# Kernel tuning notes

Measured on AMD Instinct MI355X. Metric: run time of the kernel, lower is better.

## Reference

```python
import jax, jax.numpy as jnp
import numpy as np

SPLINE_ORDER = 3
TOP_K = 2
NUM_EXPERTS = 8


def _gram_basis(x, beta_w):
    # x: (B, C, H, W) post-tanh. Returns (B, C*(S+1), H, W).
    P0 = jnp.ones_like(x)
    P1 = x
    ps = [P0, P1]
    for i in range(2, SPLINE_ORDER + 1):
        n, m = i - 1, i
        # beta(n, m) = (m+n)*(m-n)*n^2 / (m^2/(4n^2-1)) * beta_weights[n]
        beta = (m + n) * (m - n) * (n ** 2) * (4.0 * n ** 2 - 1.0) / (m ** 2) * beta_w[n]
        P2 = x * ps[-1] - beta * ps[-2]
        ps.append(P2)
    return jnp.concatenate(ps, axis=1)


def _expert(x, poly_w, beta_w):
    # tanh -> Gram polynomial basis -> SiLU -> conv2d (padding=1, stride=1)
    g = jax.nn.silu(_gram_basis(jnp.tanh(x), beta_w))
    return jax.lax.conv_general_dilated(
        g, poly_w[0], window_strides=(1, 1), padding=[(1, 1), (1, 1)],
        dimension_numbers=('NCHW', 'OIHW', 'NCHW'))


def _cv_squared(v):
    # torch.var is unbiased (ddof=1)
    return jnp.var(v, ddof=1) / (jnp.mean(v) ** 2 + 1e-10)


def reference(x, w_gate, poly_weights, beta_weights):
    B = x.shape[0]
    # gating input: global average pool -> (B, C)
    gate_x = jnp.mean(x, axis=(2, 3))
    probs = jax.nn.softmax(gate_x @ w_gate, axis=1)  # softmax BEFORE topk, as in source
    top_vals, top_idx = jax.lax.top_k(probs, TOP_K + 1)
    tk_vals = top_vals[:, :TOP_K]
    tk_idx = top_idx[:, :TOP_K]
    tk_gates = tk_vals / (jnp.sum(tk_vals, axis=1, keepdims=True) + 1e-6)
    gates = jnp.zeros_like(probs).at[jnp.arange(B)[:, None], tk_idx].set(tk_gates)
    importance = gates.sum(axis=0)
    load = jnp.sum(gates > 0, axis=0).astype(jnp.float32)  # eval-mode load
    loss = (_cv_squared(importance) + _cv_squared(load)) * 0.01
    # All experts share parameters (ModuleList([experts]*num_experts)), so
    # sum_e gates[b,e] * expert_e(x[b]) == gates.sum(1)[b] * expert(x[b]).
    y = _expert(x, poly_weights, beta_weights) * jnp.sum(gates, axis=1)[:, None, None, None]
    return y, loss


def setup_inputs() -> dict:
    key = jax.random.key(0)
    k1, k2, k3, k4 = jax.random.split(key, 4)
    x = jax.random.normal(k1, (16, 32, 192, 192), dtype=jnp.float32)
    w_gate = jax.random.normal(k2, (32, NUM_EXPERTS), dtype=jnp.float32) * 0.1
    poly_weights = jax.random.normal(k3, (1, 32, 32 * (SPLINE_ORDER + 1), 3, 3), dtype=jnp.float32) * 0.05
    beta_weights = jax.random.normal(k4, (SPLINE_ORDER + 1,), dtype=jnp.float32) * 0.01
    return {"x": x, "w_gate": w_gate, "poly_weights": poly_weights, "beta_weights": beta_weights}
```

## Files before the change

### kernel.cpp

```cpp
#include <hip/hip_runtime.h>

typedef unsigned short u16;
typedef unsigned int u32;
typedef __attribute__((ext_vector_type(8))) short bf16x8;
typedef __attribute__((ext_vector_type(4))) float f32x4;

static constexpr int B = 16, C = 32, H = 192, W = 192;
static constexpr int HW = H * W;
static constexpr int E = 8;
static constexpr int CO = 32;
static constexpr int NB = 96;
static constexpr long long NTOT = (long long)B * C * HW;
static constexpr float SILU1 = 0.7310585786300049f;

static constexpr size_t GP_OFF  = (size_t)NTOT * 2;
static constexpr size_t SCL_OFF = GP_OFF + (size_t)B * C * NB * 4;
static constexpr size_t SK_OFF  = SCL_OFF + 128;
static constexpr size_t SS_OFF  = SK_OFF + 288 * 4;
static constexpr size_t WF_OFF  = SS_OFF + 128;

__device__ inline u32 cvt_pk_bf16(float lo, float hi) {
    u32 r;
    asm("v_cvt_pk_bf16_f32 %0, %1, %2" : "=v"(r) : "v"(lo), "v"(hi));
    return r;
}
__device__ inline u16 f2b(float f) {
    u32 u = __float_as_uint(f);
    return (u16)((u + 0x7fffu + ((u >> 16) & 1u)) >> 16);
}
__device__ inline float silu_fast(float z) {
    return z * __builtin_amdgcn_rcpf(1.0f + __expf(-z));
}
__device__ inline float tanh_fast(float z) {
    float e = __expf(2.0f * z);
    return 1.0f - 2.0f * __builtin_amdgcn_rcpf(e + 1.0f);
}

__global__ __launch_bounds__(256) void stage1_prep(const float* __restrict__ x,
                                                   const float* __restrict__ pw,
                                                   u16* __restrict__ t_out,
                                                   float* __restrict__ gpart,
                                                   float* __restrict__ Sk,
                                                   float* __restrict__ Ssum,
                                                   u16* __restrict__ wfrag) {
    __shared__ float sg[2][4][16];
    __shared__ float sred[9][32][8];
    __shared__ float sks[288];
    const int blk = blockIdx.x, tid = threadIdx.x;
    if (blk < B * NB) {
        const int b = blk / NB, band = blk - (blk / NB) * NB;
        const int cp = tid & 15, part = tid >> 4;
        const size_t pbase = (size_t)b * HW + (size_t)(band * 2) * W;
        const float4* xa = (const float4*)(x + (size_t)(b * C + 2 * cp) * HW
                                             + (size_t)(band * 2) * W);
        const float4* xb = (const float4*)(x + (size_t)(b * C + 2 * cp + 1) * HW
                                             + (size_t)(band * 2) * W);
        u32* tw = (u32*)t_out;
        float s0 = 0.0f, s1 = 0.0f;
        #pragma unroll
        for (int k = 0; k < 6; ++k) {
            const int j = k * 16 + part;
            float4 a = xa[j], c = xb[j];
            s0 += (a.x + a.y) + (a.z + a.w);
            s1 += (c.x + c.y) + (c.z + c.w);
            u32 r0 = cvt_pk_bf16(tanh_fast(a.x), tanh_fast(c.x));
            u32 r1 = cvt_pk_bf16(tanh_fast(a.y), tanh_fast(c.y));
            u32 r2 = cvt_pk_bf16(tanh_fast(a.z), tanh_fast(c.z));
            u32 r3 = cvt_pk_bf16(tanh_fast(a.w), tanh_fast(c.w));
            u32* dst = tw + (pbase + (size_t)j * 4) * 16 + cp;
            dst[0] = r0; dst[16] = r1; dst[32] = r2; dst[48] = r3;
        }
        s0 += __shfl_down(s0, 32); s0 += __shfl_down(s0, 16);
        s1 += __shfl_down(s1, 32); s1 += __shfl_down(s1, 16);
        if ((part & 3) == 0) { sg[0][tid >> 6][cp] = s0; sg[1][tid >> 6][cp] = s1; }
        __syncthreads();
        if (tid < 32) {
            const int cpp = tid >> 1, o = tid & 1;
            gpart[(size_t)(b * C + tid) * NB + band] =
                (sg[o][0][cpp] + sg[o][1][cpp]) + (sg[o][2][cpp] + sg[o][3][cpp]);
        }
        return;
    }
    if (blk < B * NB + 108) {
        int j = (blk - B * NB) * 256 + tid;
        int e = j & 7, lane = (j >> 3) & 63, rest = j >> 9;
        int half = rest & 1, pt = rest >> 1;
        int p = pt / 9, tap = pt - p * 9;
        int co = half * 16 + (lane & 15);
        int ci = 32 + p * 32 + (lane >> 4) * 8 + e;
        wfrag[j] = f2b(pw[(size_t)co * 1152 + ci * 9 + tap]);
        return;
    }
    {
        const int co = tid & 31, sub = tid >> 5;
        #pragma unroll
        for (int k = 0; k < 9; ++k) {
            float s = 0.0f;
            #pragma unroll
            for (int i = 0; i < 4; ++i)
                s += pw[(size_t)co * 1152 + (sub * 4 + i) * 9 + k];
            sred[k][co][sub] = s;
        }
        __syncthreads();
        for (int j = tid; j < 288; j += 256) {
            int k = j >> 5, c = j & 31;
            float s = 0.0f;
            #pragma unroll
            for (int u = 0; u < 8; ++u) s += sred[k][c][u];
            sks[j] = s; Sk[j] = s;
        }
        __syncthreads();
        if (tid < 32) {
            float s = 0.0f;
            #pragma unroll
            for (int k = 0; k < 9; ++k) s += sks[k * 32 + tid];
            Ssum[tid] = s;
        }
    }
}

__global__ __launch_bounds__(512) void gate_k(const float* __restrict__ gpart,
                                              const float* __restrict__ wg,
                                              float* __restrict__ scl,
                                              float* __restrict__ out) {
    __shared__ float gx[B][C];
    __shared__ float lg[B][E];
    __shared__ float gt[B][E];
    const int tid = threadIdx.x;
    {
        const float4* gp = (const float4*)(gpart + (size_t)tid * NB);
        float s = 0.0f;
        #pragma unroll
        for (int k = 0; k < NB / 4; ++k) { float4 v = gp[k]; s += (v.x + v.y) + (v.z + v.w); }
        gx[tid >> 5][tid & 31] = s * (1.0f / HW);
    }
    __syncthreads();
    if (tid < B * E) {
        const int gb = tid >> 3, ge = tid & 7;
        float s = 0.0f;
        #pragma unroll
        for (int c = 0; c < C; ++c) s += gx[gb][c] * wg[c * E + ge];
        lg[gb][ge] = s;
    }
    __syncthreads();
    if (tid < B) {
        float p[E];
        float m = lg[tid][0];
        #pragma unroll
        for (int e = 1; e < E; ++e) m = fmaxf(m, lg[tid][e]);
        float sum = 0.0f;
        #pragma unroll
        for (int e = 0; e < E; ++e) { p[e] = __expf(lg[tid][e] - m); sum += p[e]; }
        float inv = 1.0f / sum;
        #pragma unroll
        for (int e = 0; e < E; ++e) p[e] *= inv;
        int i0 = 0; float v0g = p[0];
        #pragma unroll
        for (int e = 1; e < E; ++e) if (p[e] > v0g) { v0g = p[e]; i0 = e; }
        int i1 = -1; float v1g = -1.0f;
        #pragma unroll
        for (int e = 0; e < E; ++e) { if (e == i0) continue; if (p[e] > v1g) { v1g = p[e]; i1 = e; } }
        const float denom = v0g + v1g + 1e-6f;
        #pragma unroll
        for (int e = 0; e < E; ++e) gt[tid][e] = 0.0f;
        gt[tid][i0] = v0g / denom; gt[tid][i1] = v1g / denom;
        scl[tid] = gt[tid][i0] + gt[tid][i1];
    }
    __syncthreads();
    if (tid == 0) {
        float imp[E], ld[E];
        #pragma unroll
        for (int e = 0; e < E; ++e) { imp[e] = 0.0f; ld[e] = 0.0f; }
        for (int bb = 0; bb < B; ++bb)
            #pragma unroll
            for (int e = 0; e < E; ++e) {
                float g = gt[bb][e];
                imp[e] += g;
                if (g > 0.0f) ld[e] += 1.0f;
            }
        float mi = 0.0f, mld = 0.0f;
        #pragma unroll
        for (int e = 0; e < E; ++e) { mi += imp[e]; mld += ld[e]; }
        mi *= (1.0f / E); mld *= (1.0f / E);
        float vi = 0.0f, vl = 0.0f;
        #pragma unroll
        for (int e = 0; e < E; ++e) {
            float di = imp[e] - mi, dl = ld[e] - mld;
            vi += di * di; vl += dl * dl;
        }
        vi *= (1.0f / (E - 1)); vl *= (1.0f / (E - 1));
        out[NTOT] = (vi / (mi * mi + 1e-10f) + vl / (mld * mld + 1e-10f)) * 0.01f;
    }
}

static constexpr int GSTR = 40;

__global__ __launch_bounds__(256, 4) void conv_mfma(const u16* __restrict__ t_ws,
                                                 const u16* __restrict__ wfrag,
                                                 const float* __restrict__ beta_w,
                                                 const float* __restrict__ scl_ws,
                                                 const float* __restrict__ Sk,
                                                 const float* __restrict__ Ssum,
                                                 float* __restrict__ out) {
    __shared__ __align__(16) u16 gtile[324 * GSTR];

    const int b = blockIdx.z;
    const int gx0 = blockIdx.x << 4, gy0 = blockIdx.y << 4;
    const int tid = threadIdx.x;
    const int w = tid >> 6, lane = tid & 63, q = lane >> 4, ml = lane & 15;
    const float beta2 = 2.25f * beta_w[1];
    const float beta23 = beta2 + (300.0f / 9.0f) * beta_w[2];

    const int p0 = tid;
    int extra = -1;
    if ((tid & 3) == 0) extra = tid >> 2;
    else if ((tid & 63) == 1) extra = 64 + (tid >> 6);
    const int p1 = (extra >= 0) ? 256 + extra : -1;

    u32 pk0[16], pk1[16];
    bool v0, v1 = false;
    {
        int py = p0 / 18, px = p0 - py * 18;
        int gy = gy0 + py - 1, gx = gx0 + px - 1;
        v0 = (unsigned)gy < (unsigned)H && (unsigned)gx < (unsigned)W;
        if (v0) {
            const uint4* tp = (const uint4*)(t_ws + (((size_t)b * HW + (size_t)gy * W + gx) << 5));
            *(uint4*)&pk0[0]  = tp[0];
            *(uint4*)&pk0[4]  = tp[1];
            *(uint4*)&pk0[8]  = tp[2];
            *(uint4*)&pk0[12] = tp[3];
        } else {
            #pragma unroll
            for (int cc = 0; cc < 16; ++cc) pk0[cc] = 0u;
        }
        if (p1 >= 0) {
            int py1 = p1 / 18, px1 = p1 - py1 * 18;
            int gy1 = gy0 + py1 - 1, gx1 = gx0 + px1 - 1;
            v1 = (unsigned)gy1 < (unsigned)H && (unsigned)gx1 < (unsigned)W;
            if (v1) {
                const uint4* tp = (const uint4*)(t_ws + (((size_t)b * HW + (size_t)gy1 * W + gx1) << 5));
                *(uint4*)&pk1[0]  = tp[0];
                *(uint4*)&pk1[4]  = tp[1];
                *(uint4*)&pk1[8]  = tp[2];
                *(uint4*)&pk1[12] = tp[3];
            }
        }
        if (!v1) {
            #pragma unroll
            for (int cc = 0; cc < 16; ++cc) pk1[cc] = 0u;
        }
    }

    const float sc = scl_ws[b];

#define BASIS(P)                                                                \
    do {                                                                        \
        _Pragma("unroll")                                                       \
        for (int slot = 0; slot < 2; ++slot) {                                  \
            const int pix = slot ? p1 : p0;                                     \
            if (slot && p1 < 0) continue;                                       \
            const bool vv = slot ? v1 : v0;                                     \
            const u32* pk = slot ? pk1 : pk0;                                   \
            u32 r[16];                                                          \
            if (vv) {                                                           \
                _Pragma("unroll")                                               \
                for (int cc = 0; cc < 16; ++cc) {                               \
                    float tl = __uint_as_float(pk[cc] << 16);                   \
                    float th = __uint_as_float(pk[cc] & 0xffff0000u);           \
                    float ul, uh;                                               \
                    if ((P) == 0) { ul = tl; uh = th; }                         \
                    else if ((P) == 1) { ul = fmaf(tl, tl, -beta2); uh = fmaf(th, th, -beta2); } \
                    else { ul = tl * fmaf(tl, tl, -beta23); uh = th * fmaf(th, th, -beta23); } \
                    r[cc] = cvt_pk_bf16(silu_fast(ul), silu_fast(uh));          \
                }                                                               \
            } else {                                                            \
                _Pragma("unroll")                                               \
                for (int cc = 0; cc < 16; ++cc) r[cc] = 0u;                     \
            }                                                                   \
            uint4* dst = (uint4*)&gtile[pix * GSTR];                            \
            dst[0] = *(const uint4*)&r[0];                                      \
            dst[1] = *(const uint4*)&r[4];                                      \
            dst[2] = *(const uint4*)&r[8];                                      \
            dst[3] = *(const uint4*)&r[12];                                     \
        }                                                                       \
    } while (0)

    f32x4 acc[4][2];
    #pragma unroll
    for (int a = 0; a < 4; ++a) {
        acc[a][0] = (f32x4){0.0f, 0.0f, 0.0f, 0.0f};
        acc[a][1] = (f32x4){0.0f, 0.0f, 0.0f, 0.0f};
    }

#define MFMA_DX(P, DX)                                                          \
    do {                                                                        \
        const u16* wf = wfrag + (size_t)(P) * 9216;                             \
        bf16x8 bfr[3][2];                                                       \
        _Pragma("unroll")                                                       \
        for (int dyi = 0; dyi < 3; ++dyi) {                                     \
            const int tap = dyi * 3 + (DX);                                     \
            bfr[dyi][0] = *(const bf16x8*)(wf + ((size_t)(tap * 2 + 0) * 64 + lane) * 8); \
            bfr[dyi][1] = *(const bf16x8*)(wf + ((size_t)(tap * 2 + 1) * 64 + lane) * 8); \
        }                                                                       \
        bf16x8 af6[6];                                                          \
        _Pragma("unroll")                                                       \
        for (int rl = 0; rl < 6; ++rl)                                          \
            af6[rl] = *(const bf16x8*)                                          \
                &gtile[(((w << 2) + rl) * 18 + ml + (DX)) * GSTR + (q << 3)];   \
        _Pragma("unroll")                                                       \
        for (int rl = 0; rl < 6; ++rl) {                                        \
            _Pragma("unroll")                                                   \
            for (int dyi = 0; dyi < 3; ++dyi) {                                 \
                const int a = rl - dyi;                                         \
                if (a >= 0 && a < 4) {                                          \
                    acc[a][0] = __builtin_amdgcn_mfma_f32_16x16x32_bf16(af6[rl], bfr[dyi][0], acc[a][0], 0, 0, 0); \
                    acc[a][1] = __builtin_amdgcn_mfma_f32_16x16x32_bf16(af6[rl], bfr[dyi][1], acc[a][1], 0, 0, 0); \
                }                                                               \
            }                                                                   \
        }                                                                       \
    } while (0)

    BASIS(0);
    __syncthreads();
    MFMA_DX(0, 0); MFMA_DX(0, 1); MFMA_DX(0, 2);
    __syncthreads();
    BASIS(1);
    __syncthreads();
    MFMA_DX(1, 0); MFMA_DX(1, 1); MFMA_DX(1, 2);
    __syncthreads();
    BASIS(2);
    __syncthreads();
    MFMA_DX(2, 0); MFMA_DX(2, 1); MFMA_DX(2, 2);

#undef BASIS
#undef MFMA_DX

    const bool interior = (blockIdx.x > 0) && (blockIdx.x < 11) &&
                          (blockIdx.y > 0) && (blockIdx.y < 11);
    #pragma unroll
    for (int half = 0; half < 2; ++half) {
        const int co = half * 16 + ml;
        const float bfull = SILU1 * Ssum[co];
        #pragma unroll
        for (int a = 0; a < 4; ++a) {
            const int y = gy0 + (w << 2) + a;
            float ov[4];
            #pragma unroll
            for (int r = 0; r < 4; ++r) {
                float bias = bfull;
                if (!interior) {
                    const int xg = gx0 + (q << 2) + r;
                    bias = 0.0f;
                    #pragma unroll
                    for (int k = 0; k < 9; ++k) {
                        int yy = y + k / 3 - 1, xx = xg + k % 3 - 1;
                        if ((unsigned)yy < (unsigned)H && (unsigned)xx < (unsigned)W)
                            bias += Sk[k * 32 + co];
                    }
                    bias *= SILU1;
                }
                ov[r] = (acc[a][half][r] + bias) * sc;
            }
            *(float4*)&out[((size_t)(b * CO + co) * H + y) * W + gx0 + (q << 2)] = *(float4*)ov;
        }
    }
}

extern "C" void kernel_launch(void* const* d_in, const int* in_sizes, int n_in,
                              void* d_out, int out_size, void* d_ws, size_t ws_size,
                              hipStream_t stream) {
    const float* x  = (const float*)d_in[0];
    const float* wg = (const float*)d_in[1];
    const float* pw = (const float*)d_in[2];
    const float* bw = (const float*)d_in[3];
    float* out = (float*)d_out;
    char* ws = (char*)d_ws;
    u16*   t_ws  = (u16*)ws;
    float* gpart = (float*)(ws + GP_OFF);
    float* scl   = (float*)(ws + SCL_OFF);
    float* Sk    = (float*)(ws + SK_OFF);
    float* Ssum  = (float*)(ws + SS_OFF);
    u16*   wfrag = (u16*)(ws + WF_OFF);

    stage1_prep<<<dim3(B * NB + 109), 256, 0, stream>>>(x, pw, t_ws, gpart, Sk, Ssum, wfrag);
    gate_k<<<dim3(1), 512, 0, stream>>>(gpart, wg, scl, out);
    conv_mfma<<<dim3(12, 12, B), 256, 0, stream>>>(t_ws, wfrag, bw, scl, Sk, Ssum, out);
}
```

Baseline: 245.1 us.

## Fuse gating kernel into conv kernel, recomputing per-batch gate scale per block

Removes the single-block gate kernel launch. Each conv block now computes its own batch's gate scale from the pooled partial sums, and block (0,0,0) also computes the load-balancing loss. The assignment of extra halo pixels to threads is also changed so the second-slot pixels go to a contiguous range of threads. This saves one launch and its serial dependency at the cost of redundant small gating work in every block, extra shared memory, and added latency before the conv starts.

```diff
diff --git a/kernel.cpp b/kernel.cpp
--- a/kernel.cpp
+++ b/kernel.cpp
@@ -14,8 +14,7 @@
 static constexpr float SILU1 = 0.7310585786300049f;
 
 static constexpr size_t GP_OFF  = (size_t)NTOT * 2;
-static constexpr size_t SCL_OFF = GP_OFF + (size_t)B * C * NB * 4;
-static constexpr size_t SK_OFF  = SCL_OFF + 128;
+static constexpr size_t SK_OFF  = GP_OFF + (size_t)B * C * NB * 4;
 static constexpr size_t SS_OFF  = SK_OFF + 288 * 4;
 static constexpr size_t WF_OFF  = SS_OFF + 128;
 
@@ -119,90 +118,22 @@
     }
 }
 
-__global__ __launch_bounds__(512) void gate_k(const float* __restrict__ gpart,
-                                              const float* __restrict__ wg,
-                                              float* __restrict__ scl,
-                                              float* __restrict__ out) {
-    __shared__ float gx[B][C];
-    __shared__ float lg[B][E];
-    __shared__ float gt[B][E];
-    const int tid = threadIdx.x;
-    {
-        const float4* gp = (const float4*)(gpart + (size_t)tid * NB);
-        float s = 0.0f;
-        #pragma unroll
-        for (int k = 0; k < NB / 4; ++k) { float4 v = gp[k]; s += (v.x + v.y) + (v.z + v.w); }
-        gx[tid >> 5][tid & 31] = s * (1.0f / HW);
-    }
-    __syncthreads();
-    if (tid < B * E) {
-        const int gb = tid >> 3, ge = tid & 7;
-        float s = 0.0f;
-        #pragma unroll
-        for (int c = 0; c < C; ++c) s += gx[gb][c] * wg[c * E + ge];
-        lg[gb][ge] = s;
-    }
-    __syncthreads();
-    if (tid < B) {
-        float p[E];
-        float m = lg[tid][0];
-        #pragma unroll
-        for (int e = 1; e < E; ++e) m = fmaxf(m, lg[tid][e]);
-        float sum = 0.0f;
-        #pragma unroll
-        for (int e = 0; e < E; ++e) { p[e] = __expf(lg[tid][e] - m); sum += p[e]; }
-        float inv = 1.0f / sum;
-        #pragma unroll
-        for (int e = 0; e < E; ++e) p[e] *= inv;
-        int i0 = 0; float v0g = p[0];
-        #pragma unroll
-        for (int e = 1; e < E; ++e) if (p[e] > v0g) { v0g = p[e]; i0 = e; }
-        int i1 = -1; float v1g = -1.0f;
-        #pragma unroll
-        for (int e = 0; e < E; ++e) { if (e == i0) continue; if (p[e] > v1g) { v1g = p[e]; i1 = e; } }
-        const float denom = v0g + v1g + 1e-6f;
-        #pragma unroll
-        for (int e = 0; e < E; ++e) gt[tid][e] = 0.0f;
-        gt[tid][i0] = v0g / denom; gt[tid][i1] = v1g / denom;
-        scl[tid] = gt[tid][i0] + gt[tid][i1];
-    }
-    __syncthreads();
-    if (tid == 0) {
-        float imp[E], ld[E];
-        #pragma unroll
-        for (int e = 0; e < E; ++e) { imp[e] = 0.0f; ld[e] = 0.0f; }
-        for (int bb = 0; bb < B; ++bb)
-            #pragma unroll
-            for (int e = 0; e < E; ++e) {
-                float g = gt[bb][e];
-                imp[e] += g;
-                if (g > 0.0f) ld[e] += 1.0f;
-            }
-        float mi = 0.0f, mld = 0.0f;
-        #pragma unroll
-        for (int e = 0; e < E; ++e) { mi += imp[e]; mld += ld[e]; }
-        mi *= (1.0f / E); mld *= (1.0f / E);
-        float vi = 0.0f, vl = 0.0f;
-        #pragma unroll
-        for (int e = 0; e < E; ++e) {
-            float di = imp[e] - mi, dl = ld[e] - mld;
-            vi += di * di; vl += dl * dl;
-        }
-        vi *= (1.0f / (E - 1)); vl *= (1.0f / (E - 1));
-        out[NTOT] = (vi / (mi * mi + 1e-10f) + vl / (mld * mld + 1e-10f)) * 0.01f;
-    }
-}
-
 static constexpr int GSTR = 40;
 
 __global__ __launch_bounds__(256, 4) void conv_mfma(const u16* __restrict__ t_ws,
                                                  const u16* __restrict__ wfrag,
                                                  const float* __restrict__ beta_w,
-                                                 const float* __restrict__ scl_ws,
+                                                 const float* __restrict__ gpart,
+                                                 const float* __restrict__ wg,
                                                  const float* __restrict__ Sk,
                                                  const float* __restrict__ Ssum,
                                                  float* __restrict__ out) {
     __shared__ __align__(16) u16 gtile[324 * GSTR];
+    __shared__ float gxs[C];
+    __shared__ float lgs[E];
+    __shared__ float sscl;
+    __shared__ float lgx[B * C];
+    __shared__ float lgt[B * E];
 
     const int b = blockIdx.z;
     const int gx0 = blockIdx.x << 4, gy0 = blockIdx.y << 4;
@@ -212,10 +143,7 @@
     const float beta23 = beta2 + (300.0f / 9.0f) * beta_w[2];
 
     const int p0 = tid;
-    int extra = -1;
-    if ((tid & 3) == 0) extra = tid >> 2;
-    else if ((tid & 63) == 1) extra = 64 + (tid >> 6);
-    const int p1 = (extra >= 0) ? 256 + extra : -1;
+    const int p1 = (tid >= 188) ? 256 + (tid - 188) : -1;
 
     u32 pk0[16], pk1[16];
     bool v0, v1 = false;
@@ -251,7 +179,112 @@
         }
     }
 
-    const float sc = scl_ws[b];
+    {
+        const int c = tid >> 3, seg = tid & 7;
+        const float4* gp = (const float4*)(gpart + ((size_t)b * C + c) * NB + seg * 12);
+        float4 a0 = gp[0], a1 = gp[1], a2 = gp[2];
+        float s = ((a0.x + a0.y) + (a0.z + a0.w)) + ((a1.x + a1.y) + (a1.z + a1.w))
+                + ((a2.x + a2.y) + (a2.z + a2.w));
+        s += __shfl_down(s, 4, 8);
+        s += __shfl_down(s, 2, 8);
+        s += __shfl_down(s, 1, 8);
+        if (seg == 0) gxs[c] = s * (1.0f / HW);
+    }
+    __syncthreads();
+    if (tid < E) {
+        float s = 0.0f;
+        #pragma unroll
+        for (int c = 0; c < C; ++c) s += gxs[c] * wg[c * E + tid];
+        lgs[tid] = s;
+    }
+    __syncthreads();
+    if (tid == 0) {
+        float p[E];
+        float m = lgs[0];
+        #pragma unroll
+        for (int e = 1; e < E; ++e) m = fmaxf(m, lgs[e]);
+        float sum = 0.0f;
+        #pragma unroll
+        for (int e = 0; e < E; ++e) { p[e] = __expf(lgs[e] - m); sum += p[e]; }
+        float inv = 1.0f / sum;
+        #pragma unroll
+        for (int e = 0; e < E; ++e) p[e] *= inv;
+        int i0 = 0; float v0g = p[0];
+        #pragma unroll
+        for (int e = 1; e < E; ++e) if (p[e] > v0g) { v0g = p[e]; i0 = e; }
+        float v1g = -1.0f;
+        #pragma unroll
+        for (int e = 0; e < E; ++e) { if (e == i0) continue; if (p[e] > v1g) v1g = p[e]; }
+        const float denom = v0g + v1g + 1e-6f;
+        sscl = (v0g + v1g) / denom;
+    }
+
+    if (blockIdx.x == 0 && blockIdx.y == 0 && b == 0) {
+        for (int r = tid; r < B * C; r += 256) {
+            const float4* gp = (const float4*)(gpart + (size_t)r * NB);
+            float s = 0.0f;
+            #pragma unroll
+            for (int k = 0; k < NB / 4; ++k) { float4 v = gp[k]; s += (v.x + v.y) + (v.z + v.w); }
+            lgx[r] = s * (1.0f / HW);
+        }
+        __syncthreads();
+        if (tid < B) {
+            float lg[E];
+            #pragma unroll
+            for (int e = 0; e < E; ++e) {
+                float s = 0.0f;
+                #pragma unroll
+                for (int c = 0; c < C; ++c) s += lgx[tid * C + c] * wg[c * E + e];
+                lg[e] = s;
+            }
+            float p[E];
+            float m = lg[0];
+            #pragma unroll
+            for (int e = 1; e < E; ++e) m = fmaxf(m, lg[e]);
+            float sum = 0.0f;
+            #pragma unroll
+            for (int e = 0; e < E; ++e) { p[e] = __expf(lg[e] - m); sum += p[e]; }
+            float inv = 1.0f / sum;
+            #pragma unroll
+            for (int e = 0; e < E; ++e) p[e] *= inv;
+            int i0 = 0; float v0g = p[0];
+            #pragma unroll
+            for (int e = 1; e < E; ++e) if (p[e] > v0g) { v0g = p[e]; i0 = e; }
+            int i1 = -1; float v1g = -1.0f;
+            #pragma unroll
+            for (int e = 0; e < E; ++e) { if (e == i0) continue; if (p[e] > v1g) { v1g = p[e]; i1 = e; } }
+            const float denom = v0g + v1g + 1e-6f;
+            #pragma unroll
+            for (int e = 0; e < E; ++e) lgt[tid * E + e] = 0.0f;
+            lgt[tid * E + i0] = v0g / denom;
+            lgt[tid * E + i1] = v1g / denom;
+        }
+        __syncthreads();
+        if (tid == 0) {
+            float imp[E], ld[E];
+            #pragma unroll
+            for (int e = 0; e < E; ++e) { imp[e] = 0.0f; ld[e] = 0.0f; }
+            for (int bb = 0; bb < B; ++bb)
+                #pragma unroll
+                for (int e = 0; e < E; ++e) {
+                    float g = lgt[bb * E + e];
+                    imp[e] += g;
+                    if (g > 0.0f) ld[e] += 1.0f;
+                }
+            float mi = 0.0f, mld = 0.0f;
+            #pragma unroll
+            for (int e = 0; e < E; ++e) { mi += imp[e]; mld += ld[e]; }
+            mi *= (1.0f / E); mld *= (1.0f / E);
+            float vi = 0.0f, vl = 0.0f;
+            #pragma unroll
+            for (int e = 0; e < E; ++e) {
+                float di = imp[e] - mi, dl = ld[e] - mld;
+                vi += di * di; vl += dl * dl;
+            }
+            vi *= (1.0f / (E - 1)); vl *= (1.0f / (E - 1));
+            out[NTOT] = (vi / (mi * mi + 1e-10f) + vl / (mld * mld + 1e-10f)) * 0.01f;
+        }
+    }
 
 #define BASIS(P)                                                                \
     do {                                                                        \
@@ -335,6 +368,7 @@
 #undef BASIS
 #undef MFMA_DX
 
+    const float sc = sscl;
     const bool interior = (blockIdx.x > 0) && (blockIdx.x < 11) &&
                           (blockIdx.y > 0) && (blockIdx.y < 11);
     #pragma unroll
@@ -377,12 +411,10 @@
     char* ws = (char*)d_ws;
     u16*   t_ws  = (u16*)ws;
     float* gpart = (float*)(ws + GP_OFF);
-    float* scl   = (float*)(ws + SCL_OFF);
     float* Sk    = (float*)(ws + SK_OFF);
     float* Ssum  = (float*)(ws + SS_OFF);
     u16*   wfrag = (u16*)(ws + WF_OFF);
 
     stage1_prep<<<dim3(B * NB + 109), 256, 0, stream>>>(x, pw, t_ws, gpart, Sk, Ssum, wfrag);
-    gate_k<<<dim3(1), 512, 0, stream>>>(gpart, wg, scl, out);
-    conv_mfma<<<dim3(12, 12, B), 256, 0, stream>>>(t_ws, wfrag, bw, scl, Sk, Ssum, out);
-}
+    conv_mfma<<<dim3(12, 12, B), 256, 0, stream>>>(t_ws, wfrag, bw, gpart, wg, Sk, Ssum, out);
+}
```

Measured after the change: 247.9 us. Within noise of the previous version (+1.2%).
